# Kernel tuning notes

Hardware: AMD Instinct MI355X
Metric: run time of the kernel (lower is better)

Reference implementation:

```python
import jax, jax.numpy as jnp
import numpy as np

DIM = 512
NUM_HEADS = 4
SCALE = 1.0 / np.sqrt(DIM)  # note: module scales by 1/sqrt(dim), not 1/sqrt(head_dim)


def setup_inputs() -> dict:
    key = jax.random.key(0)
    k1, k2, k3, k4, k5, k6 = jax.random.split(key, 6)
    B, N, M, C = 8, 2048, 2048, DIM
    bound = 1.0 / np.sqrt(C)
    return {
        "F1": jax.random.normal(k1, (B, N, C), dtype=jnp.float32),
        "F2": jax.random.normal(k2, (B, M, C), dtype=jnp.float32),
        "W_qkv": jax.random.uniform(k3, (C, C), jnp.float32, -bound, bound),
        "b_qkv": jax.random.uniform(k4, (C,), jnp.float32, -bound, bound),
        "W_proj": jax.random.uniform(k5, (C, C), jnp.float32, -bound, bound),
        "b_proj": jax.random.uniform(k6, (C,), jnp.float32, -bound, bound),
    }


def reference(F1, F2, W_qkv, b_qkv, W_proj, b_proj):
    B, N, C = F1.shape
    M = F2.shape[1]
    H, D = NUM_HEADS, C // NUM_HEADS
    # shared qkv projection (same weights for q, k and v in the original module)
    q = (F1 @ W_qkv + b_qkv).reshape(B, N, H, D)  # queries from F1
    kv = (F2 @ W_qkv + b_qkv).reshape(B, M, H, D)  # keys == values from F2
    attn = jnp.einsum("bnhd,bmhd->bhnm", q * SCALE, kv)
    attn = jax.nn.softmax(attn, axis=-1)
    x = jnp.einsum("bhnm,bmhd->bnhd", attn, kv).reshape(B, N, C)
    return x @ W_proj + b_proj
```

## Files before the change

### kernel.cpp

```cpp
#include <hip/hip_runtime.h>
#include <math.h>


typedef __attribute__((ext_vector_type(8))) short s16x8;
typedef __attribute__((ext_vector_type(4))) float f32x4;

#define C_DIM 512
#define HDIM  128
#define NROWS 16384
#define SCALE_Q 0.04419417382415922f
#define LOG2E   1.4426950408889634f

__device__ __forceinline__ unsigned short f2bf(float f) {
    union { float f; unsigned u; } v; v.f = f;
    unsigned r = v.u + 0x7fffu + ((v.u >> 16) & 1u);
    return (unsigned short)(r >> 16);
}

__device__ __forceinline__ void async16(const void* g, void* l) {
    __builtin_amdgcn_global_load_lds(
        (const __attribute__((address_space(1))) void*)g,
        (__attribute__((address_space(3))) void*)l, 16, 0, 0);
}

__global__ __launch_bounds__(256)
void conv_bf16_2(const float* __restrict__ s0, const float* __restrict__ s1,
                 unsigned short* __restrict__ d0, unsigned short* __restrict__ d1,
                 int n8) {
    const float* src = blockIdx.y ? s1 : s0;
    unsigned short* dst = blockIdx.y ? d1 : d0;
    int i = blockIdx.x * 256 + threadIdx.x;
    if (i >= n8) return;
    float4 a = ((const float4*)src)[2 * i];
    float4 b = ((const float4*)src)[2 * i + 1];
    union { unsigned short us[8]; uint4 v; } o;
    o.us[0] = f2bf(a.x); o.us[1] = f2bf(a.y); o.us[2] = f2bf(a.z); o.us[3] = f2bf(a.w);
    o.us[4] = f2bf(b.x); o.us[5] = f2bf(b.y); o.us[6] = f2bf(b.z); o.us[7] = f2bf(b.w);
    ((uint4*)dst)[i] = o.v;
}

__global__ __launch_bounds__(256)
void wconv_t2(const float* __restrict__ W0, const float* __restrict__ W1,
              unsigned short* __restrict__ T0, unsigned short* __restrict__ T1) {
    const float* W = blockIdx.z ? W1 : W0;
    unsigned short* Wt = blockIdx.z ? T1 : T0;
    __shared__ float t[64][65];
    const int k0 = blockIdx.y * 64, n0 = blockIdx.x * 64;
    const int c = threadIdx.x & 63, r0 = threadIdx.x >> 6;
#pragma unroll
    for (int r = r0; r < 64; r += 4)
        t[r][c] = W[(size_t)(k0 + r) * C_DIM + n0 + c];
    __syncthreads();
#pragma unroll
    for (int r = r0; r < 64; r += 4)
        Wt[(size_t)(n0 + r) * C_DIM + k0 + c] = f2bf(t[c][r]);
}

__global__ __launch_bounds__(256)
void kv_transpose(const unsigned short* __restrict__ KV,
                  unsigned short* __restrict__ KVT) {
    __shared__ unsigned short t[64][66];
    const int key0 = blockIdx.x * 64;
    const int d0   = blockIdx.y * 64;
    const int bh   = blockIdx.z;
    const int b    = bh >> 2, h = bh & 3;
    const int c = threadIdx.x & 63, r0 = threadIdx.x >> 6;
    const unsigned short* src = KV + ((size_t)(b * 2048 + key0)) * C_DIM + h * HDIM + d0;
#pragma unroll
    for (int r = r0; r < 64; r += 4)
        t[r][c] = src[(size_t)r * C_DIM + c];
    __syncthreads();
    unsigned short* dst = KVT + ((size_t)(bh * HDIM + d0)) * 2048 + key0;
#pragma unroll
    for (int r = r0; r < 64; r += 4)
        dst[(size_t)r * 2048 + c] = t[c][r];
}

template <int OUT_BF16>
__global__ __launch_bounds__(256, 2)
void gemm_bt(const unsigned short* __restrict__ A,
             const unsigned short* __restrict__ Bt,
             const float* __restrict__ bias,
             void* __restrict__ Cv, float oscTop, int topRows) {
    __shared__ __align__(16) unsigned short As[2][128][64];
    __shared__ __align__(16) unsigned short Bs[2][128][64];

    const int tid  = threadIdx.x;
    const int wid  = tid >> 6;
    const int lane = tid & 63;
    const int lr   = lane & 15;
    const int quad = lane >> 4;
    const int wm   = wid >> 1;
    const int wn   = wid & 1;

    const int wg   = blockIdx.x;
    const int xcd  = wg & 7;
    const int s_   = wg >> 3;
    const int xblk = s_ & 3;
    const int y    = xcd + 8 * (s_ >> 2);
    const int rowBase = y * 128;
    const int colBase = xblk * 128;

    const int srow = lane >> 3;
    const int soff = srow * C_DIM + (((lane & 7) ^ (srow & 7)) * 8);
    const float osc = (rowBase < topRows) ? oscTop : 1.0f;

    f32x4 acc[4][4];
#pragma unroll
    for (int i = 0; i < 4; i++)
#pragma unroll
        for (int j = 0; j < 4; j++) acc[i][j] = (f32x4)0.0f;

    auto STAGE = [&](int kt, int buf) {
        const int k0 = kt * 64;
#pragma unroll
        for (int i = 0; i < 4; i++) {
            const int R = wid * 32 + i * 8;
            async16(A  + (size_t)(rowBase + R) * C_DIM + k0 + soff, &As[buf][R][0]);
            async16(Bt + (size_t)(colBase + R) * C_DIM + k0 + soff, &Bs[buf][R][0]);
        }
    };

    auto COMPUTE = [&](int buf) {
        __builtin_amdgcn_s_setprio(1);
#pragma unroll
        for (int s = 0; s < 2; s++) {
            s16x8 af[4], bf[4];
#pragma unroll
            for (int i = 0; i < 4; i++)
                af[i] = *(const s16x8*)&As[buf][wm * 64 + i * 16 + lr][((s * 4 + quad) ^ (lr & 7)) * 8];
#pragma unroll
            for (int j = 0; j < 4; j++)
                bf[j] = *(const s16x8*)&Bs[buf][wn * 64 + j * 16 + lr][((s * 4 + quad) ^ (lr & 7)) * 8];
#pragma unroll
            for (int i = 0; i < 4; i++)
#pragma unroll
                for (int j = 0; j < 4; j++)
                    acc[i][j] = __builtin_amdgcn_mfma_f32_16x16x32_bf16(af[i], bf[j], acc[i][j], 0, 0, 0);
        }
        __builtin_amdgcn_s_setprio(0);
    };

    STAGE(0, 0);
#pragma unroll 2
    for (int kt = 0; kt < 8; kt++) {
        __builtin_amdgcn_sched_barrier(0);
        __builtin_amdgcn_s_barrier();
        __builtin_amdgcn_sched_barrier(0);
        if (kt < 7) {
            STAGE(kt + 1, (kt + 1) & 1);
            asm volatile("s_waitcnt vmcnt(8)" ::: "memory");
        } else {
            asm volatile("s_waitcnt vmcnt(0)" ::: "memory");
        }
        __builtin_amdgcn_sched_barrier(0);
        __builtin_amdgcn_s_barrier();
        __builtin_amdgcn_sched_barrier(0);
        COMPUTE(kt & 1);
    }

    float bcol[4];
#pragma unroll
    for (int j = 0; j < 4; j++)
        bcol[j] = bias[colBase + wn * 64 + j * 16 + lr];
#pragma unroll
    for (int i = 0; i < 4; i++) {
#pragma unroll
        for (int j = 0; j < 4; j++) {
            const int col = colBase + wn * 64 + j * 16 + lr;
#pragma unroll
            for (int r = 0; r < 4; r++) {
                const int row = rowBase + wm * 64 + i * 16 + quad * 4 + r;
                float v = (acc[i][j][r] + bcol[j]) * osc;
                if (OUT_BF16)
                    ((unsigned short*)Cv)[(size_t)row * C_DIM + col] = f2bf(v);
                else
                    ((float*)Cv)[(size_t)row * C_DIM + col] = v;
            }
        }
    }
}

__global__ __launch_bounds__(512, 2)
void cross_attn(const unsigned short* __restrict__ Q,
                const unsigned short* __restrict__ KV,
                const unsigned short* __restrict__ KVT,
                unsigned short* __restrict__ X) {
    __shared__ __align__(16) unsigned short Kt[4][64][128];
    __shared__ __align__(16) unsigned short Vt[4][128][64];

    const int tid  = threadIdx.x;
    const int wid  = tid >> 6;
    const int lane = tid & 63;
    const int lr   = lane & 15;
    const int quad = lane >> 4;

    const int wg   = blockIdx.x;
    const int xcd  = wg & 7;
    const int slot = wg >> 3;
    const int p    = xcd + 8 * (slot & 3);
    const int xblk = slot >> 2;
    const int b    = p >> 2;
    const int h    = p & 3;
    const int hoff = h * HDIM;
    const size_t qrow0  = (size_t)b * 2048 + xblk * 256 + wid * 32;
    const size_t kvrow0 = (size_t)b * 2048;

    s16x8 qf[2][4];
#pragma unroll
    for (int i = 0; i < 2; i++)
#pragma unroll
        for (int kk = 0; kk < 4; kk++)
            qf[i][kk] = *(const s16x8*)(Q + (qrow0 + i * 16 + lr) * C_DIM + hoff + kk * 32 + quad * 8);

    const unsigned short* pK[2];
    const unsigned short* pV[2];
#pragma unroll
    for (int a = 0; a < 2; a++) {
        const int R   = wid * 8 + a * 4 + (lane >> 4);
        const int key = 32 * (R >> 5) + 8 * ((R >> 2) & 3) + 4 * ((R >> 4) & 1) + (R & 3);
        const int pp  = lane & 15;
        const int ck  = (pp & 8) | ((pp ^ (R & 7)) & 7);
        pK[a] = KV + (kvrow0 + key) * C_DIM + hoff + ck * 8;
        const int d  = wid * 16 + a * 8 + (lane >> 3);
        const int cv = (lane & 7) ^ (lane >> 3);
        pV[a] = KVT + ((size_t)((b * 4 + h) * HDIM + d)) * 2048 + cv * 8;
    }

    f32x4 O[2][8];
#pragma unroll
    for (int i = 0; i < 2; i++)
#pragma unroll
        for (int dt = 0; dt < 8; dt++) O[i][dt] = (f32x4)0.0f;
    float lacc[2];
    lacc[0] = 0.0f; lacc[1] = 0.0f;

    auto STAGE = [&](int t, int buf) {
        const size_t key0 = (size_t)t * 64;
#pragma unroll
        for (int a = 0; a < 2; a++) {
            async16(pK[a] + key0 * C_DIM, &Kt[buf][wid * 8 + a * 4][0]);
            async16(pV[a] + key0,         &Vt[buf][wid * 16 + a * 8][0]);
        }
    };

    auto COMPUTE = [&](int cur) {
        f32x4 s[2][4];
#pragma unroll
        for (int i = 0; i < 2; i++)
#pragma unroll
            for (int j = 0; j < 4; j++) s[i][j] = (f32x4)0.0f;
        __builtin_amdgcn_s_setprio(1);
#pragma unroll
        for (int kk = 0; kk < 4; kk++) {
#pragma unroll
            for (int j = 0; j < 4; j++) {
                s16x8 kf = *(const s16x8*)&Kt[cur][j * 16 + lr][((kk * 4 + quad) ^ (lr & 7)) * 8];
                s[0][j] = __builtin_amdgcn_mfma_f32_16x16x32_bf16(kf, qf[0][kk], s[0][j], 0, 0, 0);
                s[1][j] = __builtin_amdgcn_mfma_f32_16x16x32_bf16(kf, qf[1][kk], s[1][j], 0, 0, 0);
            }
        }
        __builtin_amdgcn_s_setprio(0);

        s16x8 pa[2][2];
#pragma unroll
        for (int i = 0; i < 2; i++) {
#pragma unroll
            for (int kk = 0; kk < 2; kk++) {
                float p0 = __builtin_amdgcn_exp2f(s[i][2 * kk][0]);
                float p1 = __builtin_amdgcn_exp2f(s[i][2 * kk][1]);
                float p2 = __builtin_amdgcn_exp2f(s[i][2 * kk][2]);
                float p3 = __builtin_amdgcn_exp2f(s[i][2 * kk][3]);
                float p4 = __builtin_amdgcn_exp2f(s[i][2 * kk + 1][0]);
                float p5 = __builtin_amdgcn_exp2f(s[i][2 * kk + 1][1]);
                float p6 = __builtin_amdgcn_exp2f(s[i][2 * kk + 1][2]);
                float p7 = __builtin_amdgcn_exp2f(s[i][2 * kk + 1][3]);
                lacc[i] += ((p0 + p1) + (p2 + p3)) + ((p4 + p5) + (p6 + p7));
                union { unsigned short us[8]; s16x8 v; } pu;
                pu.us[0] = f2bf(p0); pu.us[1] = f2bf(p1);
                pu.us[2] = f2bf(p2); pu.us[3] = f2bf(p3);
                pu.us[4] = f2bf(p4); pu.us[5] = f2bf(p5);
                pu.us[6] = f2bf(p6); pu.us[7] = f2bf(p7);
                pa[i][kk] = pu.v;
            }
        }

        __builtin_amdgcn_s_setprio(1);
#pragma unroll
        for (int kk = 0; kk < 2; kk++) {
#pragma unroll
            for (int dt = 0; dt < 8; dt++) {
                s16x8 vf = *(const s16x8*)&Vt[cur][dt * 16 + lr][((kk * 4 + quad) ^ (lr & 7)) * 8];
                O[0][dt] = __builtin_amdgcn_mfma_f32_16x16x32_bf16(pa[0][kk], vf, O[0][dt], 0, 0, 0);
                O[1][dt] = __builtin_amdgcn_mfma_f32_16x16x32_bf16(pa[1][kk], vf, O[1][dt], 0, 0, 0);
            }
        }
        __builtin_amdgcn_s_setprio(0);
    };

    STAGE(0, 0);
    STAGE(1, 1);

#pragma unroll 4
    for (int kt = 0; kt < 28; kt++) {
        STAGE(kt + 2, (kt + 2) & 3);
        asm volatile("s_waitcnt vmcnt(8)" ::: "memory");
        __builtin_amdgcn_sched_barrier(0);
        __builtin_amdgcn_s_barrier();
        __builtin_amdgcn_sched_barrier(0);
        COMPUTE(kt & 3);
    }
    STAGE(30, 2);
    asm volatile("s_waitcnt vmcnt(8)" ::: "memory");
    __builtin_amdgcn_sched_barrier(0);
    __builtin_amdgcn_s_barrier();
    __builtin_amdgcn_sched_barrier(0);
    COMPUTE(0);

    STAGE(31, 3);
    asm volatile("s_waitcnt vmcnt(8)" ::: "memory");
    __builtin_amdgcn_sched_barrier(0);
    __builtin_amdgcn_s_barrier();
    __builtin_amdgcn_sched_barrier(0);
    COMPUTE(1);

    asm volatile("s_waitcnt vmcnt(4)" ::: "memory");
    __builtin_amdgcn_sched_barrier(0);
    __builtin_amdgcn_s_barrier();
    __builtin_amdgcn_sched_barrier(0);
    COMPUTE(2);

    asm volatile("s_waitcnt vmcnt(0)" ::: "memory");
    __builtin_amdgcn_sched_barrier(0);
    __builtin_amdgcn_s_barrier();
    __builtin_amdgcn_sched_barrier(0);
    COMPUTE(3);

#pragma unroll
    for (int i = 0; i < 2; i++) {
        float l = lacc[i];
        l += __shfl_xor(l, 16);
        l += __shfl_xor(l, 32);
#pragma unroll
        for (int r = 0; r < 4; r++) {
            const float inv = 1.0f / __shfl(l, quad * 4 + r);
            const size_t row = (qrow0 + i * 16 + quad * 4 + r) * C_DIM + hoff;
#pragma unroll
            for (int dt = 0; dt < 8; dt++)
                X[row + dt * 16 + lr] = f2bf(O[i][dt][r] * inv);
        }
    }
}

extern "C" void kernel_launch(void* const* d_in, const int* in_sizes, int n_in,
                              void* d_out, int out_size, void* d_ws, size_t ws_size,
                              hipStream_t stream) {
    const float* F1     = (const float*)d_in[0];
    const float* F2     = (const float*)d_in[1];
    const float* W_qkv  = (const float*)d_in[2];
    const float* b_qkv  = (const float*)d_in[3];
    const float* W_proj = (const float*)d_in[4];
    const float* b_proj = (const float*)d_in[5];
    float* out = (float*)d_out;

    const size_t NC = (size_t)NROWS * C_DIM;
    unsigned short* F1b = (unsigned short*)d_ws;
    unsigned short* F2b = F1b + NC;
    unsigned short* Qw  = F2b + NC;
    unsigned short* KVw = Qw  + NC;
    unsigned short* Wqt = KVw + NC;
    unsigned short* Wpt = Wqt + C_DIM * C_DIM;
    unsigned short* Xw  = F1b;
    unsigned short* KVT = F2b;

    dim3 blk(256);

    conv_bf16_2<<<dim3(NC / 8 / 256, 2), blk, 0, stream>>>(F1, F2, F1b, F2b, (int)(NC / 8));
    wconv_t2<<<dim3(8, 8, 2), blk, 0, stream>>>(W_qkv, W_proj, Wqt, Wpt);

    gemm_bt<1><<<dim3(1024), blk, 0, stream>>>(F1b, Wqt, b_qkv, Qw, SCALE_Q * LOG2E, NROWS);
    kv_transpose<<<dim3(32, 2, 32), blk, 0, stream>>>(KVw, KVT);
    cross_attn<<<dim3(256), dim3(512), 0, stream>>>(Qw, KVw, KVT, Xw);
    gemm_bt<0><<<dim3(512), blk, 0, stream>>>(Xw, Wpt, b_proj, out, 1.0f, 0);
}
```

Baseline: 240.9 us.

## Load V fragments directly from global into registers and merge conversion kernels

The attention kernel stops staging the transposed V tile through LDS. Each wave instead loads its V MFMA operands straight from the global KVT buffer into registers at the start of each key tile, while K stays on the async LDS pipeline. The loop is restructured with adjusted vmcnt waits. This halves LDS use and the LDS read traffic for V, but it raises register pressure and exposes global-load latency inside the loop. Separately, the input bf16 conversion and weight transpose kernels are fused into one launch to save a kernel launch.

```diff
diff --git a/kernel.cpp b/kernel.cpp
--- a/kernel.cpp
+++ b/kernel.cpp
@@ -24,28 +24,29 @@
 }
 
 __global__ __launch_bounds__(256)
-void conv_bf16_2(const float* __restrict__ s0, const float* __restrict__ s1,
-                 unsigned short* __restrict__ d0, unsigned short* __restrict__ d1,
-                 int n8) {
-    const float* src = blockIdx.y ? s1 : s0;
-    unsigned short* dst = blockIdx.y ? d1 : d0;
-    int i = blockIdx.x * 256 + threadIdx.x;
-    if (i >= n8) return;
-    float4 a = ((const float4*)src)[2 * i];
-    float4 b = ((const float4*)src)[2 * i + 1];
-    union { unsigned short us[8]; uint4 v; } o;
-    o.us[0] = f2bf(a.x); o.us[1] = f2bf(a.y); o.us[2] = f2bf(a.z); o.us[3] = f2bf(a.w);
-    o.us[4] = f2bf(b.x); o.us[5] = f2bf(b.y); o.us[6] = f2bf(b.z); o.us[7] = f2bf(b.w);
-    ((uint4*)dst)[i] = o.v;
-}
-
-__global__ __launch_bounds__(256)
-void wconv_t2(const float* __restrict__ W0, const float* __restrict__ W1,
-              unsigned short* __restrict__ T0, unsigned short* __restrict__ T1) {
-    const float* W = blockIdx.z ? W1 : W0;
-    unsigned short* Wt = blockIdx.z ? T1 : T0;
+void conv_wconv(const float* __restrict__ s0, const float* __restrict__ s1,
+                unsigned short* __restrict__ d0, unsigned short* __restrict__ d1,
+                const float* __restrict__ W0, const float* __restrict__ W1,
+                unsigned short* __restrict__ T0, unsigned short* __restrict__ T1,
+                int n8) {
     __shared__ float t[64][65];
-    const int k0 = blockIdx.y * 64, n0 = blockIdx.x * 64;
+    if (blockIdx.x < 4096) {
+        const float* src = blockIdx.y ? s1 : s0;
+        unsigned short* dst = blockIdx.y ? d1 : d0;
+        int i = blockIdx.x * 256 + threadIdx.x;
+        if (i >= n8) return;
+        float4 a = ((const float4*)src)[2 * i];
+        float4 b = ((const float4*)src)[2 * i + 1];
+        union { unsigned short us[8]; uint4 v; } o;
+        o.us[0] = f2bf(a.x); o.us[1] = f2bf(a.y); o.us[2] = f2bf(a.z); o.us[3] = f2bf(a.w);
+        o.us[4] = f2bf(b.x); o.us[5] = f2bf(b.y); o.us[6] = f2bf(b.z); o.us[7] = f2bf(b.w);
+        ((uint4*)dst)[i] = o.v;
+        return;
+    }
+    const int tt = blockIdx.x - 4096;
+    const float* W = blockIdx.y ? W1 : W0;
+    unsigned short* Wt = blockIdx.y ? T1 : T0;
+    const int k0 = (tt >> 3) * 64, n0 = (tt & 7) * 64;
     const int c = threadIdx.x & 63, r0 = threadIdx.x >> 6;
 #pragma unroll
     for (int r = r0; r < 64; r += 4)
@@ -187,7 +188,6 @@
                 const unsigned short* __restrict__ KVT,
                 unsigned short* __restrict__ X) {
     __shared__ __align__(16) unsigned short Kt[4][64][128];
-    __shared__ __align__(16) unsigned short Vt[4][128][64];
 
     const int tid  = threadIdx.x;
     const int wid  = tid >> 6;
@@ -214,7 +214,6 @@
             qf[i][kk] = *(const s16x8*)(Q + (qrow0 + i * 16 + lr) * C_DIM + hoff + kk * 32 + quad * 8);
 
     const unsigned short* pK[2];
-    const unsigned short* pV[2];
 #pragma unroll
     for (int a = 0; a < 2; a++) {
         const int R   = wid * 8 + a * 4 + (lane >> 4);
@@ -222,10 +221,8 @@
         const int pp  = lane & 15;
         const int ck  = (pp & 8) | ((pp ^ (R & 7)) & 7);
         pK[a] = KV + (kvrow0 + key) * C_DIM + hoff + ck * 8;
-        const int d  = wid * 16 + a * 8 + (lane >> 3);
-        const int cv = (lane & 7) ^ (lane >> 3);
-        pV[a] = KVT + ((size_t)((b * 4 + h) * HDIM + d)) * 2048 + cv * 8;
-    }
+    }
+    const unsigned short* pVr = KVT + ((size_t)((b * 4 + h) * HDIM + lr)) * 2048 + quad * 8;
 
     f32x4 O[2][8];
 #pragma unroll
@@ -238,13 +235,32 @@
     auto STAGE = [&](int t, int buf) {
         const size_t key0 = (size_t)t * 64;
 #pragma unroll
-        for (int a = 0; a < 2; a++) {
+        for (int a = 0; a < 2; a++)
             async16(pK[a] + key0 * C_DIM, &Kt[buf][wid * 8 + a * 4][0]);
-            async16(pV[a] + key0,         &Vt[buf][wid * 16 + a * 8][0]);
-        }
     };
 
-    auto COMPUTE = [&](int cur) {
+    STAGE(0, 0);
+    STAGE(1, 1);
+
+#pragma unroll 4
+    for (int kt = 0; kt < 32; kt++) {
+        const int cur = kt & 3;
+        const size_t key0 = (size_t)kt * 64;
+
+        s16x8 vreg[16];
+#pragma unroll
+        for (int dt = 0; dt < 8; dt++)
+#pragma unroll
+            for (int kk = 0; kk < 2; kk++)
+                vreg[dt * 2 + kk] = *(const s16x8*)(pVr + (size_t)dt * 16 * 2048 + key0 + kk * 32);
+
+        if (kt < 30) STAGE(kt + 2, (kt + 2) & 3);
+        __builtin_amdgcn_sched_barrier(0);
+        asm volatile("s_waitcnt vmcnt(20)" ::: "memory");
+        __builtin_amdgcn_sched_barrier(0);
+        __builtin_amdgcn_s_barrier();
+        __builtin_amdgcn_sched_barrier(0);
+
         f32x4 s[2][4];
 #pragma unroll
         for (int i = 0; i < 2; i++)
@@ -290,51 +306,12 @@
         for (int kk = 0; kk < 2; kk++) {
 #pragma unroll
             for (int dt = 0; dt < 8; dt++) {
-                s16x8 vf = *(const s16x8*)&Vt[cur][dt * 16 + lr][((kk * 4 + quad) ^ (lr & 7)) * 8];
-                O[0][dt] = __builtin_amdgcn_mfma_f32_16x16x32_bf16(pa[0][kk], vf, O[0][dt], 0, 0, 0);
-                O[1][dt] = __builtin_amdgcn_mfma_f32_16x16x32_bf16(pa[1][kk], vf, O[1][dt], 0, 0, 0);
+                O[0][dt] = __builtin_amdgcn_mfma_f32_16x16x32_bf16(pa[0][kk], vreg[dt * 2 + kk], O[0][dt], 0, 0, 0);
+                O[1][dt] = __builtin_amdgcn_mfma_f32_16x16x32_bf16(pa[1][kk], vreg[dt * 2 + kk], O[1][dt], 0, 0, 0);
             }
         }
         __builtin_amdgcn_s_setprio(0);
-    };
-
-    STAGE(0, 0);
-    STAGE(1, 1);
-
-#pragma unroll 4
-    for (int kt = 0; kt < 28; kt++) {
-        STAGE(kt + 2, (kt + 2) & 3);
-        asm volatile("s_waitcnt vmcnt(8)" ::: "memory");
-        __builtin_amdgcn_sched_barrier(0);
-        __builtin_amdgcn_s_barrier();
-        __builtin_amdgcn_sched_barrier(0);
-        COMPUTE(kt & 3);
-    }
-    STAGE(30, 2);
-    asm volatile("s_waitcnt vmcnt(8)" ::: "memory");
-    __builtin_amdgcn_sched_barrier(0);
-    __builtin_amdgcn_s_barrier();
-    __builtin_amdgcn_sched_barrier(0);
-    COMPUTE(0);
-
-    STAGE(31, 3);
-    asm volatile("s_waitcnt vmcnt(8)" ::: "memory");
-    __builtin_amdgcn_sched_barrier(0);
-    __builtin_amdgcn_s_barrier();
-    __builtin_amdgcn_sched_barrier(0);
-    COMPUTE(1);
-
-    asm volatile("s_waitcnt vmcnt(4)" ::: "memory");
-    __builtin_amdgcn_sched_barrier(0);
-    __builtin_amdgcn_s_barrier();
-    __builtin_amdgcn_sched_barrier(0);
-    COMPUTE(2);
-
-    asm volatile("s_waitcnt vmcnt(0)" ::: "memory");
-    __builtin_amdgcn_sched_barrier(0);
-    __builtin_amdgcn_s_barrier();
-    __builtin_amdgcn_sched_barrier(0);
-    COMPUTE(3);
+    }
 
 #pragma unroll
     for (int i = 0; i < 2; i++) {
@@ -375,8 +352,8 @@
 
     dim3 blk(256);
 
-    conv_bf16_2<<<dim3(NC / 8 / 256, 2), blk, 0, stream>>>(F1, F2, F1b, F2b, (int)(NC / 8));
-    wconv_t2<<<dim3(8, 8, 2), blk, 0, stream>>>(W_qkv, W_proj, Wqt, Wpt);
+    conv_wconv<<<dim3(4160, 2), blk, 0, stream>>>(F1, F2, F1b, F2b,
+                                                  W_qkv, W_proj, Wqt, Wpt, (int)(NC / 8));
 
     gemm_bt<1><<<dim3(1024), blk, 0, stream>>>(F1b, Wqt, b_qkv, Qw, SCALE_Q * LOG2E, NROWS);
     kv_transpose<<<dim3(32, 2, 32), blk, 0, stream>>>(KVw, KVT);
```

Measured after the change: 410.9 us. +70.5%, slower.
